# Kernel tuning notes

Measured on AMD Instinct MI355X. Metric: run time of the kernel, lower is better.

Reference implementation:

```python
import jax, jax.numpy as jnp
import numpy as np

B, T, H, NH, DH, R = 2, 2048, 1024, 16, 64, 256
ALPHA = 0.6


def setup_inputs() -> dict:
    key = jax.random.key(0)
    ks = jax.random.split(key, 28)
    f32 = jnp.float32

    def nrm(k, shape, s=0.02):
        return jax.random.normal(k, shape, dtype=f32) * s

    inp = {}
    inp['x'] = jax.random.normal(ks[0], (B, T, H), dtype=f32)
    # additive causal mask [1,1,T,T]: 0 on/below diagonal, -1e9 above
    causal = jnp.tril(jnp.ones((T, T), dtype=bool))
    inp['attention_mask'] = jnp.where(causal, 0.0, -1e9).astype(f32)[None, None]
    # low-rank SVD factors for q,k,v,o: Vh [H,R], S [R] (positive), U [H,R], b [H]
    i = 1
    for name in ('q', 'k', 'v', 'o'):
        inp['Vh_' + name] = nrm(ks[i], (H, R)); i += 1
        inp['S_' + name] = jax.random.uniform(ks[i], (R,), dtype=f32, minval=0.5, maxval=1.5); i += 1
        inp['U_' + name] = nrm(ks[i], (H, R)); i += 1
        inp['b_' + name] = jnp.zeros((H,), dtype=f32); i += 1
    # full-rank weights of the original (fallback) attention: y = x @ W + b (Conv1D style)
    for name in ('q', 'k', 'v', 'o'):
        inp['W_' + name] = nrm(ks[i], (H, H)); i += 1
        inp['bf_' + name] = jnp.zeros((H,), dtype=f32); i += 1
    return inp


def _split_heads(t):
    # [B,T,H] -> [B,nH,T,dH]
    Bs, Ts, _ = t.shape
    return t.reshape(Bs, Ts, NH, DH).transpose(0, 2, 1, 3)


def _attention(Q, K, V, mask):
    q, k, v = _split_heads(Q), _split_heads(K), _split_heads(V)
    scores = jnp.einsum('bhtd,bhsd->bhts', q, k) / (DH ** 0.5)
    scores = scores + mask
    w = jax.nn.softmax(scores, axis=-1)
    ctx = jnp.einsum('bhts,bhsd->bhtd', w, v)
    Bs = ctx.shape[0]
    return ctx.transpose(0, 2, 1, 3).reshape(Bs, -1, NH * DH)


def _lowrank(x, Vh, S, U, b):
    # ((x @ Vh) * S) @ U.T + b
    return ((x @ Vh) * S) @ U.T + b


def reference(x, attention_mask,
              Vh_q, S_q, U_q, b_q, Vh_k, S_k, U_k, b_k,
              Vh_v, S_v, U_v, b_v, Vh_o, S_o, U_o, b_o,
              W_q, bf_q, W_k, bf_k, W_v, bf_v, W_o, bf_o):
    # --- low-rank SVD path ---
    Q = _lowrank(x, Vh_q, S_q, U_q, b_q)
    K = _lowrank(x, Vh_k, S_k, U_k, b_k)
    V = _lowrank(x, Vh_v, S_v, U_v, b_v)
    ctx = _attention(Q, K, V, attention_mask)
    out = _lowrank(ctx, Vh_o, S_o, U_o, b_o)
    # --- fallback: original full-rank attention ---
    Qf = x @ W_q + bf_q
    Kf = x @ W_k + bf_k
    Vf = x @ W_v + bf_v
    ctxf = _attention(Qf, Kf, Vf, attention_mask)
    fallback_out = ctxf @ W_o + bf_o
    return ALPHA * out + (1.0 - ALPHA) * fallback_out
```

## Files before the change

### kernel.cpp

```cpp
#include <hip/hip_runtime.h>
#include <hip/hip_bf16.h>

typedef __bf16 bf16_t;
typedef __bf16 bf16x4 __attribute__((ext_vector_type(4)));
typedef __bf16 bf16x8 __attribute__((ext_vector_type(8)));
typedef float f32x4 __attribute__((ext_vector_type(4)));
typedef _Float16 f16_t;
typedef _Float16 f16x4 __attribute__((ext_vector_type(4)));
typedef unsigned short us4 __attribute__((ext_vector_type(4)));

extern "C" __device__ float __ocml_native_exp2_f32(float);

#define DEVI static __device__ __forceinline__

static constexpr int TN   = 2048;
static constexpr int Hn   = 1024;
static constexpr int Rn   = 256;
static constexpr int MTOK = 4096;
static constexpr int NCAT = 6144;

static constexpr float QSCALE = 0.125f;
static constexpr float LOG2E  = 1.44269504088896340736f;
static constexpr float SOFT_OFF2 = 0.426950408889634f;

template <typename T>
DEVI void gload16(const T* g, T* l) {
    __builtin_amdgcn_global_load_lds(
        (const __attribute__((address_space(1))) void*)g,
        (__attribute__((address_space(3))) void*)l, 16, 0, 0);
}

DEVI float loadf(const void* base, int idx, bool bfm) {
    if (bfm) {
        unsigned int u = ((const unsigned short*)base)[idx];
        u <<= 16;
        return __builtin_bit_cast(float, u);
    }
    return ((const float*)base)[idx];
}
DEVI float4 loadf4(const void* base, int idx, bool bfm) {
    float4 f;
    if (bfm) {
        us4 u = *(const us4*)((const unsigned short*)base + idx);
        f.x = __builtin_bit_cast(float, (unsigned)u.x << 16);
        f.y = __builtin_bit_cast(float, (unsigned)u.y << 16);
        f.z = __builtin_bit_cast(float, (unsigned)u.z << 16);
        f.w = __builtin_bit_cast(float, (unsigned)u.w << 16);
    } else {
        f = *(const float4*)((const float*)base + idx);
    }
    return f;
}
DEVI bool detect_bf16(const void* mask) {
    return fabsf(((const float*)mask)[0]) > 1.0f;
}

struct PrepArgs {
    const void *x, *mask;
    const void *Vh[4], *S[4], *U[4];
    const void *bb[4], *bfb[4];
    const void *W[4];
    bf16_t *wdst[4];
    int wldd[4];
    float wscale[4];
    bf16_t *Xb, *Abuf, *Bbuf;
    float *biascat, *biaso;
};

__global__ __launch_bounds__(256)
void k_prep(PrepArgs a) {
    const bool bfm = detect_bf16(a.mask);
    const int bid = blockIdx.x;
    const int tid = threadIdx.x;
    __shared__ float t[32][33];
    if (bid < 1024) {
        int i = (bid * 256 + tid) * 16;
#pragma unroll
        for (int j = 0; j < 4; ++j) {
            float4 f = loadf4(a.x, i + j * 4, bfm);
            bf16x4 o;
            o[0] = (bf16_t)f.x; o[1] = (bf16_t)f.y; o[2] = (bf16_t)f.z; o[3] = (bf16_t)f.w;
            *(bf16x4*)&a.Xb[i + j * 4] = o;
        }
    } else if (bid < 2048) {
        int e4 = ((bid - 1024) * 256 + tid) * 4;
        int proj = e4 >> 18;
        int e = e4 & 262143;
        int r = e & 255;
        float sc = (proj == 0) ? QSCALE * LOG2E : ((proj == 3) ? 0.6f : 1.0f);
        float4 s4 = loadf4(a.S[proj], r, bfm);
        float4 u4 = loadf4(a.U[proj], e, bfm);
        float4 v4 = loadf4(a.Vh[proj], e, bfm);
        bf16x4 ao, bo;
        ao[0] = (bf16_t)(u4.x * s4.x * sc); ao[1] = (bf16_t)(u4.y * s4.y * sc);
        ao[2] = (bf16_t)(u4.z * s4.z * sc); ao[3] = (bf16_t)(u4.w * s4.w * sc);
        bo[0] = (bf16_t)v4.x; bo[1] = (bf16_t)v4.y; bo[2] = (bf16_t)v4.z; bo[3] = (bf16_t)v4.w;
        *(bf16x4*)&a.Abuf[e4] = ao;
        *(bf16x4*)&a.Bbuf[e4] = bo;
    } else if (bid < 2076) {
        int i = (bid - 2048) * 256 + tid;
        if (i < 1024)      a.biascat[i] = QSCALE * LOG2E * loadf(a.bb[0], i, bfm);
        else if (i < 2048) a.biascat[i] = loadf(a.bb[1], i - 1024, bfm);
        else if (i < 3072) a.biascat[i] = loadf(a.bb[2], i - 2048, bfm);
        else if (i < 4096) a.biascat[i] = QSCALE * LOG2E * loadf(a.bfb[0], i - 3072, bfm);
        else if (i < 5120) a.biascat[i] = loadf(a.bfb[1], i - 4096, bfm);
        else if (i < 6144) a.biascat[i] = loadf(a.bfb[2], i - 5120, bfm);
        else {
            int j = i - 6144;
            a.biaso[j] = 0.6f * loadf(a.bb[3], j, bfm) + 0.4f * loadf(a.bfb[3], j, bfm);
        }
    } else {
        const int tb = bid - 2076;
        const int z  = tb >> 10;
        const int rem = tb & 1023;
        const int bx = (rem & 31) * 32, by = (rem >> 5) * 32;
        const int tx = tid & 31, ty = tid >> 5;
        const void* W = a.W[z];
        bf16_t* dst = a.wdst[z];
        const int ldd = a.wldd[z];
        const float scale = a.wscale[z];
#pragma unroll
        for (int k = 0; k < 32; k += 8)
            t[ty + k][tx] = loadf(W, (by + ty + k) * Hn + bx + tx, bfm);
        __syncthreads();
#pragma unroll
        for (int k = 0; k < 32; k += 8)
            dst[(size_t)(bx + ty + k) * ldd + by + tx] = (bf16_t)(scale * t[tx][ty + k]);
    }
}

template <int MI>
DEVI void gemm_core64(const bf16_t* __restrict__ A, int lda,
                      const bf16_t* __restrict__ B, int ldb, int K,
                      bf16_t* A0, bf16_t* A1, bf16_t* B0, bf16_t* B1,
                      int bm, int bn, f32x4 (&acc)[MI][4]) {
    constexpr int MT = MI * 32;
    const int tid  = threadIdx.x;
    const int lane = tid & 63;
    const int w    = tid >> 6;
    const int wr   = (w >> 1) * (MI * 16);
    const int wc   = (w & 1) * 64;
    const int fr   = lane & 15;
    const int quad = lane >> 4;

#pragma unroll
    for (int i = 0; i < MI; ++i)
#pragma unroll
        for (int j = 0; j < 4; ++j) acc[i][j] = {0.f, 0.f, 0.f, 0.f};

    for (int kb = 0; kb < K; kb += 64) {
        __syncthreads();
        for (int u = tid; u < MT * 4; u += 256) {
            const bf16_t* as = &A[(size_t)(bm + (u >> 2)) * lda + kb + (u & 3) * 8];
            gload16(as,      &A0[u * 8]);
            gload16(as + 32, &A1[u * 8]);
        }
#pragma unroll
        for (int t = 0; t < 2; ++t) {
            int u = t * 256 + tid;
            const bf16_t* bs = &B[(size_t)(bn + (u >> 2)) * ldb + kb + (u & 3) * 8];
            gload16(bs,      &B0[u * 8]);
            gload16(bs + 32, &B1[u * 8]);
        }
        __syncthreads();

#pragma unroll
        for (int kk = 0; kk < 2; ++kk) {
            const bf16_t* Ap = kk ? A1 : A0;
            const bf16_t* Bp = kk ? B1 : B0;
            bf16x8 af[MI], bfv[4];
#pragma unroll
            for (int i = 0; i < MI; ++i)
                af[i] = *(const bf16x8*)&Ap[(wr + i * 16 + fr) * 32 + quad * 8];
#pragma unroll
            for (int j = 0; j < 4; ++j)
                bfv[j] = *(const bf16x8*)&Bp[(wc + j * 16 + fr) * 32 + quad * 8];
#pragma unroll
            for (int i = 0; i < MI; ++i)
#pragma unroll
                for (int j = 0; j < 4; ++j)
                    acc[i][j] = __builtin_amdgcn_mfma_f32_16x16x32_bf16(af[i], bfv[j], acc[i][j], 0, 0, 0);
        }
    }
}

template <int MI, bool OUT_DUAL, bool WRITE_VT>
__global__ __launch_bounds__(256)
void k_gemm(const bf16_t* __restrict__ A, int lda,
            const bf16_t* __restrict__ B, int ldb,
            void* __restrict__ C, int ldc, int K,
            const float* __restrict__ bias, const void* __restrict__ mask,
            f16_t* __restrict__ Vt_g) {
    constexpr int MT = MI * 32;
    struct GB { bf16_t A0[MT * 32]; bf16_t A1[MT * 32]; bf16_t B0[4096]; bf16_t B1[4096]; };
    union SM { GB g; f16_t Ls[WRITE_VT ? 128 * 136 : 8]; };
    __shared__ __align__(16) SM sm;

    const int tid  = threadIdx.x;
    const int lane = tid & 63;
    const int w    = tid >> 6;
    const int wr   = (w >> 1) * (MI * 16);
    const int wc   = (w & 1) * 64;
    const int bm   = blockIdx.x * MT;
    const int bn   = blockIdx.y * 128;
    const int fr   = lane & 15;
    const int quad = lane >> 4;

    f32x4 acc[MI][4];
    gemm_core64<MI>(A, lda, B, ldb, K, sm.g.A0, sm.g.A1, sm.g.B0, sm.g.B1, bm, bn, acc);

    if constexpr (WRITE_VT) {
        const bool isV = (bn >= 2048 && bn < 3072) || (bn >= 5120);
        if (isV) {
            const int pth = (bn >= 5120) ? 1 : 0;
            const int colrel = bn - (pth ? 5120 : 2048);
            const int bb = bm >> 11;
            const int R0 = (pth * 32 + bb * 16 + (colrel >> 6)) * 64;
            const int tloc = bm & 2047;
            __syncthreads();
#pragma unroll
            for (int i = 0; i < MI; ++i) {
                const int t0 = wr + i * 16 + quad * 4;
#pragma unroll
                for (int j = 0; j < 4; ++j) {
                    const int c = wc + j * 16 + fr;
                    const float bv = bias[bn + c];
#pragma unroll
                    for (int r = 0; r < 4; ++r)
                        sm.Ls[c * 136 + t0 + r] = (f16_t)(acc[i][j][r] + bv);
                }
            }
            __syncthreads();
            const int c = tid >> 1, seg = tid & 1;
            f16_t* dst = &Vt_g[(size_t)(R0 + c) * TN + tloc + seg * 64];
            const f16_t* src = &sm.Ls[c * 136 + seg * 64];
#pragma unroll
            for (int e = 0; e < 8; ++e)
                *(uint4*)&dst[e * 8] = *(const uint4*)&src[e * 8];
            return;
        }
    }

    bool bfm = false;
    if constexpr (OUT_DUAL) bfm = detect_bf16(mask);
#pragma unroll
    for (int i = 0; i < MI; ++i) {
        const int row0 = bm + wr + i * 16 + quad * 4;
#pragma unroll
        for (int j = 0; j < 4; ++j) {
            const int col = bn + wc + j * 16 + fr;
            const float bv = bias ? bias[col] : 0.f;
#pragma unroll
            for (int r = 0; r < 4; ++r) {
                float v = acc[i][j][r] + bv;
                size_t ci = (size_t)(row0 + r) * ldc + col;
                if constexpr (OUT_DUAL) {
                    if (bfm) ((unsigned short*)C)[ci] = __builtin_bit_cast(unsigned short, (bf16_t)v);
                    else     ((float*)C)[ci] = v;
                } else {
                    ((bf16_t*)C)[ci] = (bf16_t)v;
                }
            }
        }
    }
}

__global__ __launch_bounds__(256)
void k_gemm_small4(const bf16_t* __restrict__ Abuf, const bf16_t* __restrict__ Bbuf,
                   bf16_t* __restrict__ Wcat, bf16_t* __restrict__ WoT) {
    __shared__ __align__(16) bf16_t A0[64 * 32], A1[64 * 32], B0[4096], B1[4096];
    const int z = blockIdx.z;
    const bf16_t* A = Abuf + (size_t)z * Hn * Rn;
    const bf16_t* B = Bbuf + (size_t)z * Hn * Rn;
    bf16_t* C = (z < 3) ? (Wcat + (size_t)z * Hn * Hn) : WoT;
    const int ldc = (z < 3) ? Hn : 2048;

    const int bm = blockIdx.x * 64, bn = blockIdx.y * 128;
    f32x4 acc[2][4];
    gemm_core64<2>(A, Rn, B, Rn, Rn, A0, A1, B0, B1, bm, bn, acc);

    const int lane = threadIdx.x & 63;
    const int w    = threadIdx.x >> 6;
    const int wr   = (w >> 1) * 32;
    const int wc   = (w & 1) * 64;
    const int fr   = lane & 15;
    const int quad = lane >> 4;
#pragma unroll
    for (int i = 0; i < 2; ++i)
#pragma unroll
        for (int j = 0; j < 4; ++j)
#pragma unroll
            for (int r = 0; r < 4; ++r)
                C[(size_t)(bm + wr + i * 16 + quad * 4 + r) * ldc + bn + wc + j * 16 + fr]
                    = (bf16_t)acc[i][j][r];
}

__global__ __launch_bounds__(256, 4)
void k_flash6(const bf16_t* __restrict__ Y, const f16_t* __restrict__ Vt_g,
              bf16_t* __restrict__ Ctx) {
    const int id   = blockIdx.x;
    const int inst = id & 63;
    const int slot = (id >> 6) & 3;
    const int rnd  = id >> 8;
    const int qt2  = (rnd == 0) ? 15 - slot
                   : (rnd == 1) ? 11 - slot
                   : (rnd == 2) ? 4 + slot
                                : slot;
    const int p = inst >> 5, b = (inst >> 4) & 1, h = inst & 15;

    const int tid  = threadIdx.x;
    const int lane = tid & 63;
    const int w    = tid >> 6;
    const int fr   = lane & 15;
    const int quad = lane >> 4;

    const int rowbase = b * TN;
    const int qbase   = qt2 * 128;
    const int qcol = p * 3072 + h * 64;
    const int kcol = qcol + 1024;
    const int ccol = p * 1024 + h * 64;

    __shared__ __align__(16) bf16_t Kb[2][2][64 * 32];
    __shared__ __align__(16) f16_t  Vb[2][64 * 64];

    const int r64 = tid >> 2;
    const int c8s = (((tid & 3) ^ ((tid >> 4) & 3)) * 8);
    const int ksw = (quad ^ ((fr >> 2) & 3)) * 8;

    size_t vsrc[2];
#pragma unroll
    for (int t = 0; t < 2; ++t) {
        int pp = w * 128 + t * 64 + lane;
        int d  = pp >> 3;
        vsrc[t] = (size_t)(inst * 64 + d) * TN + ((((pp & 7) - d) & 7) * 8);
    }

    f16x4 ones;
#pragma unroll
    for (int j = 0; j < 4; ++j) ones[j] = (f16_t)1.0f;

    const f32x4 off4 = {-SOFT_OFF2, -SOFT_OFF2, -SOFT_OFF2, -SOFT_OFF2};

    bf16x8 qf[2][2];
#pragma unroll
    for (int s = 0; s < 2; ++s) {
        const size_t qrow = (size_t)(rowbase + qbase + s * 64 + w * 16 + fr) * NCAT + qcol;
        qf[s][0] = *(const bf16x8*)&Y[qrow + quad * 8];
        qf[s][1] = *(const bf16x8*)&Y[qrow + 32 + quad * 8];
    }

    f32x4 o[2][4], lacc[2];
#pragma unroll
    for (int s = 0; s < 2; ++s) {
        lacc[s] = {0.f, 0.f, 0.f, 0.f};
#pragma unroll
        for (int db = 0; db < 4; ++db) o[s][db] = {0.f, 0.f, 0.f, 0.f};
    }

    const int t0 = (quad >> 1) + (fr & 7);
    const int h4 = (quad & 1) * 4;
    int voff[4];
#pragma unroll
    for (int nb = 0; nb < 4; ++nb) voff[nb] = ((nb * 2 + t0) & 7) * 8;

    const int kl = quad * 4;
    const int ql = w * 16 + fr;

    const int kmax = 2 * qt2 + 1;

    auto stage = [&](int kt, int bsel) {
        const bf16_t* ksrc = &Y[(size_t)(rowbase + kt * 64 + r64) * NCAT + kcol + c8s];
        gload16(ksrc,      &Kb[bsel][0][tid * 8]);
        gload16(ksrc + 32, &Kb[bsel][1][tid * 8]);
#pragma unroll
        for (int t = 0; t < 2; ++t)
            gload16(&Vt_g[vsrc[t] + kt * 64], &Vb[bsel][(w * 128 + t * 64 + lane) * 8]);
    };

    stage(0, 0);

    for (int kt = 0; kt <= kmax; ++kt) {
        const int cur = kt & 1;
        __syncthreads();
        if (kt < kmax) stage(kt + 1, cur ^ 1);

        const bool a0 = (kt < kmax);

        f16x4 pf[2][4];
#pragma unroll
        for (int nb = 0; nb < 4; ++nb) {
            const int ka = (nb * 16 + fr) * 32 + ksw;
            bf16x8 kf0 = *(const bf16x8*)&Kb[cur][0][ka];
            bf16x8 kf1 = *(const bf16x8*)&Kb[cur][1][ka];
#pragma unroll
            for (int s = 0; s < 2; ++s) {
                if (s == 0 && !a0) continue;
                f32x4 t4 = __builtin_amdgcn_mfma_f32_16x16x32_bf16(kf0, qf[s][0], off4, 0, 0, 0);
                t4 = __builtin_amdgcn_mfma_f32_16x16x32_bf16(kf1, qf[s][1], t4, 0, 0, 0);
                if (kt == 2 * qt2 + s) {
#pragma unroll
                    for (int r = 0; r < 4; ++r)
                        if (nb * 16 + kl + r > ql) t4[r] = -1e30f;
                }
                auto lo = __builtin_amdgcn_cvt_pkrtz(__ocml_native_exp2_f32(t4[0]),
                                                     __ocml_native_exp2_f32(t4[1]));
                auto hi = __builtin_amdgcn_cvt_pkrtz(__ocml_native_exp2_f32(t4[2]),
                                                     __ocml_native_exp2_f32(t4[3]));
                pf[s][nb] = __builtin_bit_cast(f16x4, __builtin_shufflevector(lo, hi, 0, 1, 2, 3));
            }
        }

#pragma unroll
        for (int s = 0; s < 2; ++s) {
            if (s == 0 && !a0) continue;
#pragma unroll
            for (int nb = 0; nb < 4; ++nb)
                lacc[s] = __builtin_amdgcn_mfma_f32_16x16x16f16(pf[s][nb], ones, lacc[s], 0, 0, 0);
        }

#pragma unroll
        for (int db = 0; db < 4; ++db) {
            const int vbase = (db * 16 + fr) * 64 + h4;
            f16x4 vf[4];
#pragma unroll
            for (int nb = 0; nb < 4; ++nb)
                vf[nb] = *(const f16x4*)&Vb[cur][vbase + voff[nb]];
#pragma unroll
            for (int nb = 0; nb < 4; ++nb) {
                o[1][db] = __builtin_amdgcn_mfma_f32_16x16x16f16(pf[1][nb], vf[nb], o[1][db], 0, 0, 0);
                if (a0)
                    o[0][db] = __builtin_amdgcn_mfma_f32_16x16x16f16(pf[0][nb], vf[nb], o[0][db], 0, 0, 0);
            }
        }
    }

#pragma unroll
    for (int s = 0; s < 2; ++s)
#pragma unroll
        for (int r = 0; r < 4; ++r) {
            const float inv = 1.0f / lacc[s][r];
            const size_t trow = (size_t)(rowbase + qbase + s * 64 + w * 16 + quad * 4 + r);
#pragma unroll
            for (int db = 0; db < 4; ++db)
                Ctx[trow * 2048 + ccol + db * 16 + fr] = (bf16_t)(o[s][db][r] * inv);
        }
}

extern "C" void kernel_launch(void* const* d_in, const int* in_sizes, int n_in,
                              void* d_out, int out_size, void* d_ws, size_t ws_size,
                              hipStream_t stream) {
    const void* x    = d_in[0];
    const void* mask = d_in[1];
    const void* Vh[4] = { d_in[2],  d_in[6],  d_in[10], d_in[14] };
    const void* Sp[4] = { d_in[3],  d_in[7],  d_in[11], d_in[15] };
    const void* Up[4] = { d_in[4],  d_in[8],  d_in[12], d_in[16] };
    const void* bb[4] = { d_in[5],  d_in[9],  d_in[13], d_in[17] };
    const void* Wp[4] = { d_in[18], d_in[20], d_in[22], d_in[24] };
    const void* bf[4] = { d_in[19], d_in[21], d_in[23], d_in[25] };

    char* ws = (char*)d_ws;
    size_t off = 0;
    auto alloc = [&](size_t bytes) -> void* {
        void* p = ws + off;
        off = (off + bytes + 255) & ~(size_t)255;
        return p;
    };
    bf16_t* Xb      = (bf16_t*)alloc((size_t)MTOK * Hn * 2);
    bf16_t* Wcat    = (bf16_t*)alloc((size_t)NCAT * Hn * 2);
    bf16_t* Yb      = (bf16_t*)alloc((size_t)MTOK * NCAT * 2);
    bf16_t* Ctx     = (bf16_t*)alloc((size_t)MTOK * 2048 * 2);
    bf16_t* WoT     = (bf16_t*)alloc((size_t)Hn * 2048 * 2);
    f16_t*  Vt_g    = (f16_t*)alloc((size_t)64 * 64 * TN * 2);
    bf16_t* Abuf    = (bf16_t*)alloc((size_t)4 * Hn * Rn * 2);
    bf16_t* Bbuf    = (bf16_t*)alloc((size_t)4 * Hn * Rn * 2);
    float*  biascat = (float*)alloc(NCAT * 4);
    float*  biaso   = (float*)alloc(Hn * 4);

    PrepArgs pa;
    pa.x = x; pa.mask = mask;
    for (int i = 0; i < 4; ++i) {
        pa.Vh[i] = Vh[i]; pa.S[i] = Sp[i]; pa.U[i] = Up[i];
        pa.bb[i] = bb[i]; pa.bfb[i] = bf[i];
        pa.W[i] = Wp[i];
    }
    for (int i = 0; i < 3; ++i) {
        pa.wdst[i] = Wcat + (size_t)(3 * Hn + i * Hn) * Hn;
        pa.wldd[i] = Hn;
        pa.wscale[i] = (i == 0) ? QSCALE * LOG2E : 1.0f;
    }
    pa.wdst[3] = WoT + 1024; pa.wldd[3] = 2048; pa.wscale[3] = 0.4f;
    pa.Xb = Xb; pa.Abuf = Abuf; pa.Bbuf = Bbuf; pa.biascat = biascat; pa.biaso = biaso;
    k_prep<<<6172, 256, 0, stream>>>(pa);

    k_gemm_small4<<<dim3(16, 8, 4), 256, 0, stream>>>(Abuf, Bbuf, Wcat, WoT);

    k_gemm<4, false, true><<<dim3(32, 48), 256, 0, stream>>>(
        Xb, Hn, Wcat, Hn, Yb, NCAT, Hn, biascat, nullptr, Vt_g);

    k_flash6<<<1024, 256, 0, stream>>>(Yb, Vt_g, Ctx);

    k_gemm<4, true, false><<<dim3(32, 8), 256, 0, stream>>>(
        Ctx, 2048, WoT, 2048, d_out, Hn, 2048, biaso, mask, nullptr);
}
```

Before: 295.2 us.

## Compute low-rank QKV as factored two-stage GEMM instead of materializing dense weights

The low-rank Q/K/V projections are no longer expanded into dense 1024x1024 weight matrices before the main GEMM. Instead x is multiplied by the scaled, transposed Vh factors to produce a rank-256 intermediate Z, and Z is then multiplied by U inside the QKV kernel. The low-rank Q/K/V blocks thus run with K=256 instead of K=1024, cutting that portion's FLOPs by about a factor of four, while the full-rank blocks are interleaved in the same grid. The cost is an extra intermediate buffer, an extra GEMM over all tokens (x@Vh) and an added rounding step through bf16 for Z.

```diff
diff --git a/kernel.cpp b/kernel.cpp
--- a/kernel.cpp
+++ b/kernel.cpp
@@ -63,7 +63,7 @@
     bf16_t *wdst[4];
     int wldd[4];
     float wscale[4];
-    bf16_t *Xb, *Abuf, *Bbuf;
+    bf16_t *Xb, *Abuf, *Bbuf, *Ubuf, *VhTs;
     float *biascat, *biaso;
 };
 
@@ -82,23 +82,49 @@
             o[0] = (bf16_t)f.x; o[1] = (bf16_t)f.y; o[2] = (bf16_t)f.z; o[3] = (bf16_t)f.w;
             *(bf16x4*)&a.Xb[i + j * 4] = o;
         }
-    } else if (bid < 2048) {
+    } else if (bid < 1280) {
         int e4 = ((bid - 1024) * 256 + tid) * 4;
-        int proj = e4 >> 18;
-        int e = e4 & 262143;
-        int r = e & 255;
-        float sc = (proj == 0) ? QSCALE * LOG2E : ((proj == 3) ? 0.6f : 1.0f);
-        float4 s4 = loadf4(a.S[proj], r, bfm);
-        float4 u4 = loadf4(a.U[proj], e, bfm);
-        float4 v4 = loadf4(a.Vh[proj], e, bfm);
+        int r = e4 & 255;
+        float4 s4 = loadf4(a.S[3], r, bfm);
+        float4 u4 = loadf4(a.U[3], e4, bfm);
+        float4 v4 = loadf4(a.Vh[3], e4, bfm);
         bf16x4 ao, bo;
-        ao[0] = (bf16_t)(u4.x * s4.x * sc); ao[1] = (bf16_t)(u4.y * s4.y * sc);
-        ao[2] = (bf16_t)(u4.z * s4.z * sc); ao[3] = (bf16_t)(u4.w * s4.w * sc);
+        ao[0] = (bf16_t)(u4.x * s4.x * 0.6f); ao[1] = (bf16_t)(u4.y * s4.y * 0.6f);
+        ao[2] = (bf16_t)(u4.z * s4.z * 0.6f); ao[3] = (bf16_t)(u4.w * s4.w * 0.6f);
         bo[0] = (bf16_t)v4.x; bo[1] = (bf16_t)v4.y; bo[2] = (bf16_t)v4.z; bo[3] = (bf16_t)v4.w;
         *(bf16x4*)&a.Abuf[e4] = ao;
         *(bf16x4*)&a.Bbuf[e4] = bo;
-    } else if (bid < 2076) {
-        int i = (bid - 2048) * 256 + tid;
+    } else if (bid < 1472) {
+        int i = ((bid - 1280) * 256 + tid) * 16;
+        int proj = i >> 18;
+        int e = i & 262143;
+#pragma unroll
+        for (int j = 0; j < 4; ++j) {
+            float4 f = loadf4(a.U[proj], e + j * 4, bfm);
+            bf16x4 o;
+            o[0] = (bf16_t)f.x; o[1] = (bf16_t)f.y; o[2] = (bf16_t)f.z; o[3] = (bf16_t)f.w;
+            *(bf16x4*)&a.Ubuf[i + j * 4] = o;
+        }
+    } else if (bid < 2240) {
+        const int tb = bid - 1472;
+        const int proj = tb >> 8;
+        const int rem = tb & 255;
+        const int bx = (rem & 7) * 32;
+        const int by = (rem >> 3) * 32;
+        const int tx = tid & 31, ty = tid >> 5;
+        const float sc = (proj == 0) ? QSCALE * LOG2E : 1.0f;
+        bf16_t* dst = a.VhTs + (size_t)proj * Rn * Hn;
+#pragma unroll
+        for (int k = 0; k < 32; k += 8)
+            t[ty + k][tx] = loadf(a.Vh[proj], (by + ty + k) * Rn + bx + tx, bfm);
+        __syncthreads();
+#pragma unroll
+        for (int k = 0; k < 32; k += 8) {
+            const int r = bx + ty + k;
+            dst[(size_t)r * Hn + by + tx] = (bf16_t)(sc * loadf(a.S[proj], r, bfm) * t[tx][ty + k]);
+        }
+    } else if (bid < 2268) {
+        int i = (bid - 2240) * 256 + tid;
         if (i < 1024)      a.biascat[i] = QSCALE * LOG2E * loadf(a.bb[0], i, bfm);
         else if (i < 2048) a.biascat[i] = loadf(a.bb[1], i - 1024, bfm);
         else if (i < 3072) a.biascat[i] = loadf(a.bb[2], i - 2048, bfm);
@@ -110,7 +136,7 @@
             a.biaso[j] = 0.6f * loadf(a.bb[3], j, bfm) + 0.4f * loadf(a.bfb[3], j, bfm);
         }
     } else {
-        const int tb = bid - 2076;
+        const int tb = bid - 2268;
         const int z  = tb >> 10;
         const int rem = tb & 1023;
         const int bx = (rem & 31) * 32, by = (rem >> 5) * 32;
@@ -184,17 +210,14 @@
     }
 }
 
-template <int MI, bool OUT_DUAL, bool WRITE_VT>
+template <int MI, bool OUT_DUAL>
 __global__ __launch_bounds__(256)
 void k_gemm(const bf16_t* __restrict__ A, int lda,
             const bf16_t* __restrict__ B, int ldb,
             void* __restrict__ C, int ldc, int K,
-            const float* __restrict__ bias, const void* __restrict__ mask,
-            f16_t* __restrict__ Vt_g) {
+            const float* __restrict__ bias, const void* __restrict__ mask) {
     constexpr int MT = MI * 32;
-    struct GB { bf16_t A0[MT * 32]; bf16_t A1[MT * 32]; bf16_t B0[4096]; bf16_t B1[4096]; };
-    union SM { GB g; f16_t Ls[WRITE_VT ? 128 * 136 : 8]; };
-    __shared__ __align__(16) SM sm;
+    __shared__ __align__(16) bf16_t A0[MT * 32], A1[MT * 32], B0[4096], B1[4096];
 
     const int tid  = threadIdx.x;
     const int lane = tid & 63;
@@ -207,39 +230,7 @@
     const int quad = lane >> 4;
 
     f32x4 acc[MI][4];
-    gemm_core64<MI>(A, lda, B, ldb, K, sm.g.A0, sm.g.A1, sm.g.B0, sm.g.B1, bm, bn, acc);
-
-    if constexpr (WRITE_VT) {
-        const bool isV = (bn >= 2048 && bn < 3072) || (bn >= 5120);
-        if (isV) {
-            const int pth = (bn >= 5120) ? 1 : 0;
-            const int colrel = bn - (pth ? 5120 : 2048);
-            const int bb = bm >> 11;
-            const int R0 = (pth * 32 + bb * 16 + (colrel >> 6)) * 64;
-            const int tloc = bm & 2047;
-            __syncthreads();
-#pragma unroll
-            for (int i = 0; i < MI; ++i) {
-                const int t0 = wr + i * 16 + quad * 4;
-#pragma unroll
-                for (int j = 0; j < 4; ++j) {
-                    const int c = wc + j * 16 + fr;
-                    const float bv = bias[bn + c];
-#pragma unroll
-                    for (int r = 0; r < 4; ++r)
-                        sm.Ls[c * 136 + t0 + r] = (f16_t)(acc[i][j][r] + bv);
-                }
-            }
-            __syncthreads();
-            const int c = tid >> 1, seg = tid & 1;
-            f16_t* dst = &Vt_g[(size_t)(R0 + c) * TN + tloc + seg * 64];
-            const f16_t* src = &sm.Ls[c * 136 + seg * 64];
-#pragma unroll
-            for (int e = 0; e < 8; ++e)
-                *(uint4*)&dst[e * 8] = *(const uint4*)&src[e * 8];
-            return;
-        }
-    }
+    gemm_core64<MI>(A, lda, B, ldb, K, A0, A1, B0, B1, bm, bn, acc);
 
     bool bfm = false;
     if constexpr (OUT_DUAL) bfm = detect_bf16(mask);
@@ -266,18 +257,24 @@
 }
 
 __global__ __launch_bounds__(256)
-void k_gemm_small4(const bf16_t* __restrict__ Abuf, const bf16_t* __restrict__ Bbuf,
-                   bf16_t* __restrict__ Wcat, bf16_t* __restrict__ WoT) {
+void k_small(const bf16_t* __restrict__ Abuf_o, const bf16_t* __restrict__ Bbuf_o,
+             const bf16_t* __restrict__ Xb, const bf16_t* __restrict__ VhTs,
+             bf16_t* __restrict__ Z, bf16_t* __restrict__ WoT) {
     __shared__ __align__(16) bf16_t A0[64 * 32], A1[64 * 32], B0[4096], B1[4096];
-    const int z = blockIdx.z;
-    const bf16_t* A = Abuf + (size_t)z * Hn * Rn;
-    const bf16_t* B = Bbuf + (size_t)z * Hn * Rn;
-    bf16_t* C = (z < 3) ? (Wcat + (size_t)z * Hn * Hn) : WoT;
-    const int ldc = (z < 3) ? Hn : 2048;
-
-    const int bm = blockIdx.x * 64, bn = blockIdx.y * 128;
+    const int x = blockIdx.x, y = blockIdx.y;
+
+    const bf16_t* A; const bf16_t* B; bf16_t* C;
+    int lda, ldb, ldc, K, bm, bn;
+    if (y < 6) {
+        A = Xb;   lda = Hn;  B = VhTs; ldb = Hn;  C = Z;   ldc = 768;  K = Hn;
+        bm = x * 64; bn = y * 128;
+    } else {
+        A = Abuf_o; lda = Rn; B = Bbuf_o; ldb = Rn; C = WoT; ldc = 2048; K = Rn;
+        bm = (x & 15) * 64; bn = ((y - 6) * 4 + (x >> 4)) * 128;
+    }
+
     f32x4 acc[2][4];
-    gemm_core64<2>(A, Rn, B, Rn, Rn, A0, A1, B0, B1, bm, bn, acc);
+    gemm_core64<2>(A, lda, B, ldb, K, A0, A1, B0, B1, bm, bn, acc);
 
     const int lane = threadIdx.x & 63;
     const int w    = threadIdx.x >> 6;
@@ -293,6 +290,87 @@
             for (int r = 0; r < 4; ++r)
                 C[(size_t)(bm + wr + i * 16 + quad * 4 + r) * ldc + bn + wc + j * 16 + fr]
                     = (bf16_t)acc[i][j][r];
+}
+
+__global__ __launch_bounds__(256)
+void k_qkv(const bf16_t* __restrict__ Z, const bf16_t* __restrict__ Ubuf,
+           const bf16_t* __restrict__ Xb, const bf16_t* __restrict__ Wfull,
+           bf16_t* __restrict__ Yb, const float* __restrict__ bias,
+           f16_t* __restrict__ Vt_g) {
+    union SM { struct { bf16_t A0[128 * 32], A1[128 * 32], B0[4096], B1[4096]; } g;
+               f16_t Ls[128 * 136]; };
+    __shared__ __align__(16) SM sm;
+
+    const int tid  = threadIdx.x;
+    const int lane = tid & 63;
+    const int w    = tid >> 6;
+    const int wr   = (w >> 1) * 64;
+    const int wc   = (w & 1) * 64;
+    const int bm   = blockIdx.x * 128;
+    const int fr   = lane & 15;
+    const int quad = lane >> 4;
+
+    const int yy   = blockIdx.y;
+    const bool lrb = (yy & 1);
+    const int half = yy >> 1;
+    const int bn   = lrb ? half * 128 : 3072 + half * 128;
+
+    const bf16_t* A; const bf16_t* B;
+    int lda, ldb, K, bnb;
+    if (lrb) {
+        const int proj = bn >> 10;
+        A = Z + proj * 256;  lda = 768;  K = 256;
+        B = Ubuf + (size_t)proj * (Hn * Rn); ldb = Rn; bnb = bn & 1023;
+    } else {
+        A = Xb; lda = Hn; K = Hn;
+        B = Wfull; ldb = Hn; bnb = bn - 3072;
+    }
+
+    f32x4 acc[4][4];
+    gemm_core64<4>(A, lda, B, ldb, K, sm.g.A0, sm.g.A1, sm.g.B0, sm.g.B1, bm, bnb, acc);
+
+    const bool isV = (bn >= 2048 && bn < 3072) || (bn >= 5120);
+    if (isV) {
+        const int pth = (bn >= 5120) ? 1 : 0;
+        const int colrel = bn - (pth ? 5120 : 2048);
+        const int bb = bm >> 11;
+        const int R0 = (pth * 32 + bb * 16 + (colrel >> 6)) * 64;
+        const int tloc = bm & 2047;
+        __syncthreads();
+#pragma unroll
+        for (int i = 0; i < 4; ++i) {
+            const int t0 = wr + i * 16 + quad * 4;
+#pragma unroll
+            for (int j = 0; j < 4; ++j) {
+                const int c = wc + j * 16 + fr;
+                const float bv = bias[bn + c];
+#pragma unroll
+                for (int r = 0; r < 4; ++r)
+                    sm.Ls[c * 136 + t0 + r] = (f16_t)(acc[i][j][r] + bv);
+            }
+        }
+        __syncthreads();
+        const int c = tid >> 1, seg = tid & 1;
+        f16_t* dst = &Vt_g[(size_t)(R0 + c) * TN + tloc + seg * 64];
+        const f16_t* src = &sm.Ls[c * 136 + seg * 64];
+#pragma unroll
+        for (int e = 0; e < 8; ++e)
+            *(uint4*)&dst[e * 8] = *(const uint4*)&src[e * 8];
+        return;
+    }
+
+#pragma unroll
+    for (int i = 0; i < 4; ++i) {
+        const int row0 = bm + wr + i * 16 + quad * 4;
+#pragma unroll
+        for (int j = 0; j < 4; ++j) {
+            const int col = bn + wc + j * 16 + fr;
+            const float bv = bias[col];
+#pragma unroll
+            for (int r = 0; r < 4; ++r)
+                Yb[(size_t)(row0 + r) * NCAT + col] = (bf16_t)(acc[i][j][r] + bv);
+        }
+    }
 }
 
 __global__ __launch_bounds__(256, 4)
@@ -466,13 +544,16 @@
         return p;
     };
     bf16_t* Xb      = (bf16_t*)alloc((size_t)MTOK * Hn * 2);
-    bf16_t* Wcat    = (bf16_t*)alloc((size_t)NCAT * Hn * 2);
+    bf16_t* Wfull   = (bf16_t*)alloc((size_t)3 * Hn * Hn * 2);
     bf16_t* Yb      = (bf16_t*)alloc((size_t)MTOK * NCAT * 2);
     bf16_t* Ctx     = (bf16_t*)alloc((size_t)MTOK * 2048 * 2);
     bf16_t* WoT     = (bf16_t*)alloc((size_t)Hn * 2048 * 2);
     f16_t*  Vt_g    = (f16_t*)alloc((size_t)64 * 64 * TN * 2);
-    bf16_t* Abuf    = (bf16_t*)alloc((size_t)4 * Hn * Rn * 2);
-    bf16_t* Bbuf    = (bf16_t*)alloc((size_t)4 * Hn * Rn * 2);
+    bf16_t* Zbuf    = (bf16_t*)alloc((size_t)MTOK * 768 * 2);
+    bf16_t* Ubuf    = (bf16_t*)alloc((size_t)3 * Hn * Rn * 2);
+    bf16_t* VhTs    = (bf16_t*)alloc((size_t)3 * Rn * Hn * 2);
+    bf16_t* Abuf    = (bf16_t*)alloc((size_t)Hn * Rn * 2);
+    bf16_t* Bbuf    = (bf16_t*)alloc((size_t)Hn * Rn * 2);
     float*  biascat = (float*)alloc(NCAT * 4);
     float*  biaso   = (float*)alloc(Hn * 4);
 
@@ -484,21 +565,22 @@
         pa.W[i] = Wp[i];
     }
     for (int i = 0; i < 3; ++i) {
-        pa.wdst[i] = Wcat + (size_t)(3 * Hn + i * Hn) * Hn;
+        pa.wdst[i] = Wfull + (size_t)i * Hn * Hn;
         pa.wldd[i] = Hn;
         pa.wscale[i] = (i == 0) ? QSCALE * LOG2E : 1.0f;
     }
     pa.wdst[3] = WoT + 1024; pa.wldd[3] = 2048; pa.wscale[3] = 0.4f;
-    pa.Xb = Xb; pa.Abuf = Abuf; pa.Bbuf = Bbuf; pa.biascat = biascat; pa.biaso = biaso;
-    k_prep<<<6172, 256, 0, stream>>>(pa);
-
-    k_gemm_small4<<<dim3(16, 8, 4), 256, 0, stream>>>(Abuf, Bbuf, Wcat, WoT);
-
-    k_gemm<4, false, true><<<dim3(32, 48), 256, 0, stream>>>(
-        Xb, Hn, Wcat, Hn, Yb, NCAT, Hn, biascat, nullptr, Vt_g);
+    pa.Xb = Xb; pa.Abuf = Abuf; pa.Bbuf = Bbuf; pa.Ubuf = Ubuf; pa.VhTs = VhTs;
+    pa.biascat = biascat; pa.biaso = biaso;
+    k_prep<<<6364, 256, 0, stream>>>(pa);
+
+    k_small<<<dim3(64, 8), 256, 0, stream>>>(Abuf, Bbuf, Xb, VhTs, Zbuf, WoT);
+
+    k_qkv<<<dim3(32, 48), 256, 0, stream>>>(
+        Zbuf, Ubuf, Xb, Wfull, Yb, biascat, Vt_g);
 
     k_flash6<<<1024, 256, 0, stream>>>(Yb, Vt_g, Ctx);
 
-    k_gemm<4, true, false><<<dim3(32, 8), 256, 0, stream>>>(
-        Ctx, 2048, WoT, 2048, d_out, Hn, 2048, biaso, mask, nullptr);
-}
+    k_gemm<4, true><<<dim3(32, 8), 256, 0, stream>>>(
+        Ctx, 2048, WoT, 2048, d_out, Hn, 2048, biaso, mask);
+}
```

Result: no change. 300.5 us (+1.8%).
